# Performance work log

Measured on AMD Instinct MI355X. Metric: run time of the kernel, lower is better.

The kernel has to match this reference:

```python
import jax, jax.numpy as jnp
import numpy as np

D_MODEL = 1024
N_HEADS = 16
HEAD_DIM = D_MODEL // N_HEADS
ROPE_BASE = 10000.0
B, S = 2, 2048


def _rope_cos_sin(seq_len):
    inv_freq = 1.0 / (ROPE_BASE ** (jnp.arange(0, HEAD_DIM, 2, dtype=jnp.float32) / HEAD_DIM))
    t = jnp.arange(seq_len, dtype=jnp.float32)
    freqs = jnp.outer(t, inv_freq)                 # [S, HEAD_DIM/2]
    emb = jnp.concatenate([freqs, freqs], axis=-1)  # [S, HEAD_DIM]
    return jnp.cos(emb), jnp.sin(emb)


def _apply_rope(x, cos, sin):
    # x: [B, H, S, D]; cos/sin: [S, D]
    x1 = x[..., ::2]
    x2 = x[..., 1::2]
    return jnp.concatenate(
        [x1 * cos[..., ::2] - x2 * sin[..., ::2],
         x1 * sin[..., 1::2] + x2 * cos[..., 1::2]], axis=-1)


def setup_inputs() -> dict:
    key = jax.random.key(0)
    ks = jax.random.split(key, 5)
    std = 1.0 / np.sqrt(D_MODEL)
    x = jax.random.normal(ks[0], (B, S, D_MODEL), dtype=jnp.float32)
    Wq = jax.random.normal(ks[1], (D_MODEL, D_MODEL), dtype=jnp.float32) * std
    Wk = jax.random.normal(ks[2], (D_MODEL, D_MODEL), dtype=jnp.float32) * std
    Wv = jax.random.normal(ks[3], (D_MODEL, D_MODEL), dtype=jnp.float32) * std
    Wo = jax.random.normal(ks[4], (D_MODEL, D_MODEL), dtype=jnp.float32) * std
    attn_mask = jnp.tril(jnp.ones((S, S), dtype=jnp.int32))  # 0 = masked (causal)
    return {"x": x, "Wq": Wq, "Wk": Wk, "Wv": Wv, "Wo": Wo, "attn_mask": attn_mask}


def reference(x, Wq, Wk, Wv, Wo, attn_mask):
    b, s, _ = x.shape
    scale = 1.0 / np.sqrt(HEAD_DIM)
    # torch Linear: y = x @ W.T
    q = (x @ Wq.T).reshape(b, s, N_HEADS, HEAD_DIM).transpose(0, 2, 1, 3)
    k = (x @ Wk.T).reshape(b, s, N_HEADS, HEAD_DIM).transpose(0, 2, 1, 3)
    v = (x @ Wv.T).reshape(b, s, N_HEADS, HEAD_DIM).transpose(0, 2, 1, 3)
    cos, sin = _rope_cos_sin(s)
    q = _apply_rope(q, cos, sin)
    k = _apply_rope(k, cos, sin)
    scores = jnp.einsum('bhqd,bhkd->bhqk', q, k) * scale  # [B,H,S,S]
    scores = jnp.where(attn_mask == 0, -jnp.inf, scores)
    attn = jax.nn.softmax(scores, axis=-1)
    out = jnp.einsum('bhqk,bhkd->bhqd', attn, v)
    out = out.transpose(0, 2, 1, 3).reshape(b, s, D_MODEL)
    return out @ Wo.T
```

## Files before the change

### kernel.cpp

```cpp
#include <hip/hip_runtime.h>
#include <hip/hip_bf16.h>
#include <cstdint>

#define SEQ 2048
#define NH  16
#define HD  64
#define DM  1024
#define BATCH 2

typedef unsigned short ushort_t;
typedef __attribute__((ext_vector_type(8))) short short8;
typedef __attribute__((ext_vector_type(4))) float f32x4;

__device__ __forceinline__ ushort_t f2bf(float f){
  __hip_bfloat16 h = __float2bfloat16(f);
  return *reinterpret_cast<ushort_t*>(&h);
}
__device__ __forceinline__ ushort_t f2bf_fast(float f){
  uint32_t u = __float_as_uint(f);
  u += 0x7FFF + ((u >> 16) & 1);
  return (ushort_t)(u >> 16);
}

__global__ __launch_bounds__(256) void rope_tab_kernel(float* __restrict__ tab){
  int idx = blockIdx.x * 256 + threadIdx.x;
  int t = idx >> 5, j = idx & 31;
  float invf = exp2f(-(float)j * 0.41524101186092033f);
  float sn, cn;
  sincosf((float)t * invf, &sn, &cn);
  tab[2*idx]   = cn;
  tab[2*idx+1] = sn;
}

__global__ __launch_bounds__(256) void cvt_kernel(
    const float* __restrict__ x,  const float* __restrict__ Wq,
    const float* __restrict__ Wk, const float* __restrict__ Wv,
    const float* __restrict__ Wo,
    ushort_t* __restrict__ xb,  ushort_t* __restrict__ wqb,
    ushort_t* __restrict__ wkb, ushort_t* __restrict__ wvb,
    ushort_t* __restrict__ wob)
{
  int f = blockIdx.x * 256 + threadIdx.x;
  const float* s; ushort_t* d; int off;
  if(f < (1<<20)){ s = x; d = xb; off = f; }
  else{
    int r = f - (1<<20);
    int w = r >> 18;
    off = r & ((1<<18)-1);
    s = (w==0)?Wq:(w==1)?Wk:(w==2)?Wv:Wo;
    d = (w==0)?wqb:(w==1)?wkb:(w==2)?wvb:wob;
  }
  float4 v = *reinterpret_cast<const float4*>(s + (size_t)off*4);
  ushort_t t[4] = {f2bf(v.x), f2bf(v.y), f2bf(v.z), f2bf(v.w)};
  *reinterpret_cast<uint2*>(d + (size_t)off*4) = *reinterpret_cast<const uint2*>(t);
}

__device__ __forceinline__ void gemm_core_bf16(
    const ushort_t* __restrict__ A, const ushort_t* __restrict__ B,
    ushort_t* As, ushort_t* Bs, int m0, int n0, f32x4 acc[4][4])
{
  const int tid  = threadIdx.x;
  const int lane = tid & 63;
  const int wave = tid >> 6;
  const int quad = lane >> 4, l16 = lane & 15;
  const int wm = (wave >> 1) * 64, wn = (wave & 1) * 64;
  for(int k0 = 0; k0 < DM; k0 += 32){
    #pragma unroll
    for(int u = 0; u < 2; u++){
      int idx = tid + u * 256;
      int row = idx >> 2, seg = idx & 3;
      *reinterpret_cast<uint4*>(&As[row*40 + seg*8]) =
        *reinterpret_cast<const uint4*>(&A[(size_t)(m0+row)*DM + k0 + seg*8]);
      *reinterpret_cast<uint4*>(&Bs[row*40 + seg*8]) =
        *reinterpret_cast<const uint4*>(&B[(size_t)(n0+row)*DM + k0 + seg*8]);
    }
    __syncthreads();
    short8 af[4], bf[4];
    #pragma unroll
    for(int mt=0;mt<4;mt++) af[mt] = *reinterpret_cast<const short8*>(&As[(wm+mt*16+l16)*40 + quad*8]);
    #pragma unroll
    for(int nt=0;nt<4;nt++) bf[nt] = *reinterpret_cast<const short8*>(&Bs[(wn+nt*16+l16)*40 + quad*8]);
    #pragma unroll
    for(int mt=0;mt<4;mt++)
      #pragma unroll
      for(int nt=0;nt<4;nt++)
        acc[mt][nt] = __builtin_amdgcn_mfma_f32_16x16x32_bf16(af[mt], bf[nt], acc[mt][nt], 0, 0, 0);
    __syncthreads();
  }
}
__device__ __forceinline__ void gemm_core_f32(
    const float* __restrict__ A, const float* __restrict__ B,
    ushort_t* As, ushort_t* Bs, int m0, int n0, f32x4 acc[4][4])
{
  const int tid  = threadIdx.x;
  const int lane = tid & 63;
  const int wave = tid >> 6;
  const int quad = lane >> 4, l16 = lane & 15;
  const int wm = (wave >> 1) * 64, wn = (wave & 1) * 64;
  for(int k0 = 0; k0 < DM; k0 += 32){
    #pragma unroll
    for(int u = 0; u < 4; u++){
      int idx = tid + u * 256;
      int row = idx >> 3, seg = idx & 7;
      float4 av = *reinterpret_cast<const float4*>(&A[(size_t)(m0+row)*DM + k0 + seg*4]);
      float4 bv = *reinterpret_cast<const float4*>(&B[(size_t)(n0+row)*DM + k0 + seg*4]);
      ushort_t at[4] = {f2bf(av.x), f2bf(av.y), f2bf(av.z), f2bf(av.w)};
      ushort_t bt[4] = {f2bf(bv.x), f2bf(bv.y), f2bf(bv.z), f2bf(bv.w)};
      *reinterpret_cast<uint2*>(&As[row*40 + seg*4]) = *reinterpret_cast<const uint2*>(at);
      *reinterpret_cast<uint2*>(&Bs[row*40 + seg*4]) = *reinterpret_cast<const uint2*>(bt);
    }
    __syncthreads();
    short8 af[4], bf[4];
    #pragma unroll
    for(int mt=0;mt<4;mt++) af[mt] = *reinterpret_cast<const short8*>(&As[(wm+mt*16+l16)*40 + quad*8]);
    #pragma unroll
    for(int nt=0;nt<4;nt++) bf[nt] = *reinterpret_cast<const short8*>(&Bs[(wn+nt*16+l16)*40 + quad*8]);
    #pragma unroll
    for(int mt=0;mt<4;mt++)
      #pragma unroll
      for(int nt=0;nt<4;nt++)
        acc[mt][nt] = __builtin_amdgcn_mfma_f32_16x16x32_bf16(af[mt], bf[nt], acc[mt][nt], 0, 0, 0);
    __syncthreads();
  }
}

__device__ __forceinline__ void qkv_epilogue(
    int z, int m0, int n0, f32x4 acc[4][4], const float* __restrict__ tab,
    ushort_t* __restrict__ Q, ushort_t* __restrict__ Ko, ushort_t* __restrict__ Vt)
{
  const int tid  = threadIdx.x;
  const int lane = tid & 63;
  const int wave = tid >> 6;
  const int quad = lane >> 4, l16 = lane & 15;
  const int wm = (wave >> 1) * 64, wn = (wave & 1) * 64;
  if(z < 2){
    ushort_t* outp = (z == 0) ? Q : Ko;
    const float qscale = (z == 0) ? 0.125f : 1.0f;
    #pragma unroll
    for(int nt=0;nt<4;nt++){
      int n  = n0 + wn + nt*16 + l16;
      int h  = n >> 6, dh = n & 63;
      int j  = dh & 31;
      int outd = (dh >> 1) + (dh & 1) * 32;
      bool even = (dh & 1) == 0;
      #pragma unroll
      for(int mt=0;mt<4;mt++){
        #pragma unroll
        for(int r=0;r<4;r++){
          int m = m0 + wm + mt*16 + quad*4 + r;
          int b = m >> 11, s = m & 2047;
          float v = acc[mt][nt][r];
          float p = __shfl_xor(v, 1);
          float2 cs = *reinterpret_cast<const float2*>(&tab[(s*32 + j)*2]);
          float o = even ? (v * cs.x - p * cs.y) : (p * cs.y + v * cs.x);
          outp[((size_t)(b*NH + h)*SEQ + s)*HD + outd] = f2bf(o * qscale);
        }
      }
    }
  } else {
    #pragma unroll
    for(int nt=0;nt<4;nt++){
      int n = n0 + wn + nt*16 + l16;
      int h = n >> 6, dh = n & 63;
      #pragma unroll
      for(int mt=0;mt<4;mt++){
        #pragma unroll
        for(int r=0;r<4;r++){
          int m = m0 + wm + mt*16 + quad*4 + r;
          int b = m >> 11, s = m & 2047;
          Vt[((size_t)(b*NH + h)*HD + dh)*SEQ + s] = f2bf(acc[mt][nt][r]);
        }
      }
    }
  }
}

__global__ __launch_bounds__(256) void qkv_bf16_kernel(
    const ushort_t* __restrict__ xb,
    const ushort_t* __restrict__ wqb, const ushort_t* __restrict__ wkb,
    const ushort_t* __restrict__ wvb, const float* __restrict__ tab,
    ushort_t* __restrict__ Q, ushort_t* __restrict__ Ko, ushort_t* __restrict__ Vt)
{
  const int z = blockIdx.z;
  const ushort_t* W = (z == 0) ? wqb : (z == 1) ? wkb : wvb;
  const int m0 = blockIdx.x * 128, n0 = blockIdx.y * 128;
  __shared__ __align__(16) char smem[20480];
  ushort_t* As = (ushort_t*)smem;
  ushort_t* Bs = (ushort_t*)(smem + 10240);
  f32x4 acc[4][4];
  #pragma unroll
  for(int i=0;i<4;i++)
    #pragma unroll
    for(int j=0;j<4;j++) acc[i][j] = (f32x4){0.f,0.f,0.f,0.f};
  gemm_core_bf16(xb, W, As, Bs, m0, n0, acc);
  qkv_epilogue(z, m0, n0, acc, tab, Q, Ko, Vt);
}

__global__ __launch_bounds__(256) void qkv_f32_kernel(
    const float* __restrict__ x,
    const float* __restrict__ Wq, const float* __restrict__ Wk,
    const float* __restrict__ Wv, const float* __restrict__ tab,
    ushort_t* __restrict__ Q, ushort_t* __restrict__ Ko, ushort_t* __restrict__ Vt)
{
  const int z = blockIdx.z;
  const float* W = (z == 0) ? Wq : (z == 1) ? Wk : Wv;
  const int m0 = blockIdx.x * 128, n0 = blockIdx.y * 128;
  __shared__ __align__(16) char smem[20480];
  ushort_t* As = (ushort_t*)smem;
  ushort_t* Bs = (ushort_t*)(smem + 10240);
  f32x4 acc[4][4];
  #pragma unroll
  for(int i=0;i<4;i++)
    #pragma unroll
    for(int j=0;j<4;j++) acc[i][j] = (f32x4){0.f,0.f,0.f,0.f};
  gemm_core_f32(x, W, As, Bs, m0, n0, acc);
  qkv_epilogue(z, m0, n0, acc, tab, Q, Ko, Vt);
}

__global__ __launch_bounds__(256) void attn_kernel(
    ushort_t* __restrict__ Qbuf, const ushort_t* __restrict__ K,
    const ushort_t* __restrict__ Vt)
{
  const int bh = blockIdx.x;
  const int y  = blockIdx.y;
  const int g  = (y < 8) ? (15 - y) : (y - 8);
  const int T  = 2*(g+1);
  const int tid  = threadIdx.x;
  const int lane = tid & 63;
  const int wave = tid >> 6;
  const int quad = lane >> 4, l16 = lane & 15;

  ushort_t*       Qp = Qbuf + (size_t)bh * SEQ * HD;
  const ushort_t* Kp = K    + (size_t)bh * SEQ * HD;
  const ushort_t* Vp = Vt   + (size_t)bh * HD * SEQ;

  __shared__ __align__(16) ushort_t Ks[64*72];
  __shared__ __align__(16) ushort_t Vs[64*72];
  __shared__ __align__(16) ushort_t Pl[4][32*72];
  ushort_t* pl = &Pl[wave][0];

  const int srow0 = tid >> 3;
  const int scol  = (tid & 7) * 8;

  const int q0w = 128*g + 32*wave;

  short8 qf[2][2];
  #pragma unroll
  for(int s=0;s<2;s++)
    #pragma unroll
    for(int kk=0;kk<2;kk++)
      qf[s][kk] = *reinterpret_cast<const short8*>(&Qp[(size_t)(q0w + 16*s + l16)*HD + kk*32 + quad*8]);

  f32x4 oacc[2][4];
  #pragma unroll
  for(int s=0;s<2;s++)
    #pragma unroll
    for(int dt=0;dt<4;dt++) oacc[s][dt] = (f32x4){0.f,0.f,0.f,0.f};
  float llane[2] = {0.f, 0.f};

  uint4 kreg[2], vreg[2];
  #pragma unroll
  for(int u=0;u<2;u++){
    int row = srow0 + u*32;
    kreg[u] = *reinterpret_cast<const uint4*>(&Kp[(size_t)row*HD + scol]);
    vreg[u] = *reinterpret_cast<const uint4*>(&Vp[(size_t)row*SEQ + scol]);
  }

  for(int t = 0; t < T; t++){
    const int kv0 = t * 64;

    __syncthreads();
    #pragma unroll
    for(int u=0;u<2;u++){
      int row = srow0 + u*32;
      *reinterpret_cast<uint4*>(&Ks[row*72 + scol]) = kreg[u];
      *reinterpret_cast<uint4*>(&Vs[row*72 + scol]) = vreg[u];
    }
    __syncthreads();

    if(t < T-1){
      #pragma unroll
      for(int u=0;u<2;u++){
        int row = srow0 + u*32;
        kreg[u] = *reinterpret_cast<const uint4*>(&Kp[(size_t)(kv0 + 64 + row)*HD + scol]);
        vreg[u] = *reinterpret_cast<const uint4*>(&Vp[(size_t)row*SEQ + kv0 + 64 + scol]);
      }
    }

    short8 kf[4][2], vf[4][2];
    #pragma unroll
    for(int nt=0;nt<4;nt++)
      #pragma unroll
      for(int kk=0;kk<2;kk++)
        kf[nt][kk] = *reinterpret_cast<const short8*>(&Ks[(nt*16 + l16)*72 + kk*32 + quad*8]);
    #pragma unroll
    for(int dt=0;dt<4;dt++)
      #pragma unroll
      for(int kk=0;kk<2;kk++)
        vf[dt][kk] = *reinterpret_cast<const short8*>(&Vs[(dt*16 + l16)*72 + kk*32 + quad*8]);

    #pragma unroll
    for(int s=0;s<2;s++){
      f32x4 sacc[4];
      #pragma unroll
      for(int nt=0;nt<4;nt++) sacc[nt] = (f32x4){0.f,0.f,0.f,0.f};
      #pragma unroll
      for(int kk=0;kk<2;kk++)
        #pragma unroll
        for(int nt=0;nt<4;nt++)
          sacc[nt] = __builtin_amdgcn_mfma_f32_16x16x32_bf16(kf[nt][kk], qf[s][kk], sacc[nt], 0,0,0);

      const int q_abs = q0w + 16*s + l16;
      const bool maskable = (kv0 + 63 > q0w + 16*s);
      float pv[4][4];
      #pragma unroll
      for(int nt=0;nt<4;nt++)
        #pragma unroll
        for(int r=0;r<4;r++){
          float sv = sacc[nt][r];
          if(maskable){
            int kv_abs = kv0 + nt*16 + quad*4 + r;
            sv = (kv_abs > q_abs) ? -1e30f : sv;
          }
          float p = __expf(sv);
          pv[nt][r] = p;
          llane[s] += p;
        }

      asm volatile("" ::: "memory");
      #pragma unroll
      for(int nt=0;nt<4;nt++){
        uint32_t lo = (uint32_t)f2bf_fast(pv[nt][0]) | ((uint32_t)f2bf_fast(pv[nt][1]) << 16);
        uint32_t hi = (uint32_t)f2bf_fast(pv[nt][2]) | ((uint32_t)f2bf_fast(pv[nt][3]) << 16);
        uint2 pk; pk.x = lo; pk.y = hi;
        *reinterpret_cast<uint2*>(&pl[(16*s + l16)*72 + nt*16 + quad*4]) = pk;
      }
      asm volatile("s_waitcnt lgkmcnt(0)" ::: "memory");

      #pragma unroll
      for(int kk=0;kk<2;kk++){
        short8 pf = *reinterpret_cast<const short8*>(&pl[(16*s + l16)*72 + kk*32 + quad*8]);
        #pragma unroll
        for(int dt=0;dt<4;dt++)
          oacc[s][dt] = __builtin_amdgcn_mfma_f32_16x16x32_bf16(vf[dt][kk], pf, oacc[s][dt], 0,0,0);
      }
    }
  }

  #pragma unroll
  for(int s=0;s<2;s++){
    float lt = llane[s];
    lt += __shfl_xor(lt, 16);
    lt += __shfl_xor(lt, 32);
    float inv = 1.0f / lt;
    #pragma unroll
    for(int dt=0;dt<4;dt++){
      uint32_t lo = (uint32_t)f2bf_fast(oacc[s][dt][0] * inv) | ((uint32_t)f2bf_fast(oacc[s][dt][1] * inv) << 16);
      uint32_t hi = (uint32_t)f2bf_fast(oacc[s][dt][2] * inv) | ((uint32_t)f2bf_fast(oacc[s][dt][3] * inv) << 16);
      uint2 pk; pk.x = lo; pk.y = hi;
      *reinterpret_cast<uint2*>(&Qp[(size_t)(q0w + 16*s + l16)*HD + dt*16 + quad*4]) = pk;
    }
  }
}

__global__ __launch_bounds__(256) void out_proj_bf16_kernel(
    const ushort_t* __restrict__ ctx, const ushort_t* __restrict__ wob,
    float* __restrict__ out)
{
  const int m0 = blockIdx.x * 128, n0 = blockIdx.y * 128;
  __shared__ __align__(16) ushort_t As[128*40];
  __shared__ __align__(16) ushort_t Bs[128*40];
  const int tid  = threadIdx.x;
  const int lane = tid & 63;
  const int wave = tid >> 6;
  const int quad = lane >> 4, l16 = lane & 15;
  const int wm = (wave >> 1) * 64, wn = (wave & 1) * 64;

  f32x4 acc[4][4];
  #pragma unroll
  for(int i=0;i<4;i++)
    #pragma unroll
    for(int j=0;j<4;j++) acc[i][j] = (f32x4){0.f,0.f,0.f,0.f};

  for(int k0 = 0; k0 < DM; k0 += 32){
    const int head = k0 >> 6, off = k0 & 63;
    #pragma unroll
    for(int u = 0; u < 2; u++){
      int idx = tid + u * 256;
      int row = idx >> 2, seg = idx & 3;
      int m = m0 + row, b = m >> 11, s = m & 2047;
      *reinterpret_cast<uint4*>(&As[row*40 + seg*8]) =
        *reinterpret_cast<const uint4*>(&ctx[((size_t)(b*NH + head)*SEQ + s)*HD + off + seg*8]);
      *reinterpret_cast<uint4*>(&Bs[row*40 + seg*8]) =
        *reinterpret_cast<const uint4*>(&wob[(size_t)(n0+row)*DM + k0 + seg*8]);
    }
    __syncthreads();
    short8 af[4], bf[4];
    #pragma unroll
    for(int mt=0;mt<4;mt++) af[mt] = *reinterpret_cast<const short8*>(&As[(wm+mt*16+l16)*40 + quad*8]);
    #pragma unroll
    for(int nt=0;nt<4;nt++) bf[nt] = *reinterpret_cast<const short8*>(&Bs[(wn+nt*16+l16)*40 + quad*8]);
    #pragma unroll
    for(int mt=0;mt<4;mt++)
      #pragma unroll
      for(int nt=0;nt<4;nt++)
        acc[mt][nt] = __builtin_amdgcn_mfma_f32_16x16x32_bf16(af[mt], bf[nt], acc[mt][nt], 0, 0, 0);
    __syncthreads();
  }
  #pragma unroll
  for(int mt=0;mt<4;mt++)
    #pragma unroll
    for(int nt=0;nt<4;nt++)
      #pragma unroll
      for(int r=0;r<4;r++){
        int m = m0 + wm + mt*16 + quad*4 + r;
        int n = n0 + wn + nt*16 + l16;
        out[(size_t)m*DM + n] = acc[mt][nt][r];
      }
}

__global__ __launch_bounds__(256) void out_proj_f32_kernel(
    const ushort_t* __restrict__ ctx, const float* __restrict__ Wo,
    float* __restrict__ out)
{
  const int m0 = blockIdx.x * 128, n0 = blockIdx.y * 128;
  __shared__ __align__(16) ushort_t As[128*40];
  __shared__ __align__(16) ushort_t Bs[128*40];
  const int tid  = threadIdx.x;
  const int lane = tid & 63;
  const int wave = tid >> 6;
  const int quad = lane >> 4, l16 = lane & 15;
  const int wm = (wave >> 1) * 64, wn = (wave & 1) * 64;

  f32x4 acc[4][4];
  #pragma unroll
  for(int i=0;i<4;i++)
    #pragma unroll
    for(int j=0;j<4;j++) acc[i][j] = (f32x4){0.f,0.f,0.f,0.f};

  for(int k0 = 0; k0 < DM; k0 += 32){
    const int head = k0 >> 6, off = k0 & 63;
    #pragma unroll
    for(int u = 0; u < 2; u++){
      int idx = tid + u * 256;
      int row = idx >> 2, seg = idx & 3;
      int m = m0 + row, b = m >> 11, s = m & 2047;
      *reinterpret_cast<uint4*>(&As[row*40 + seg*8]) =
        *reinterpret_cast<const uint4*>(&ctx[((size_t)(b*NH + head)*SEQ + s)*HD + off + seg*8]);
    }
    #pragma unroll
    for(int u = 0; u < 4; u++){
      int idx = tid + u * 256;
      int row = idx >> 3, seg = idx & 7;
      float4 bv = *reinterpret_cast<const float4*>(&Wo[(size_t)(n0+row)*DM + k0 + seg*4]);
      ushort_t bt[4] = {f2bf(bv.x), f2bf(bv.y), f2bf(bv.z), f2bf(bv.w)};
      *reinterpret_cast<uint2*>(&Bs[row*40 + seg*4]) = *reinterpret_cast<const uint2*>(bt);
    }
    __syncthreads();
    short8 af[4], bf[4];
    #pragma unroll
    for(int mt=0;mt<4;mt++) af[mt] = *reinterpret_cast<const short8*>(&As[(wm+mt*16+l16)*40 + quad*8]);
    #pragma unroll
    for(int nt=0;nt<4;nt++) bf[nt] = *reinterpret_cast<const short8*>(&Bs[(wn+nt*16+l16)*40 + quad*8]);
    #pragma unroll
    for(int mt=0;mt<4;mt++)
      #pragma unroll
      for(int nt=0;nt<4;nt++)
        acc[mt][nt] = __builtin_amdgcn_mfma_f32_16x16x32_bf16(af[mt], bf[nt], acc[mt][nt], 0, 0, 0);
    __syncthreads();
  }
  #pragma unroll
  for(int mt=0;mt<4;mt++)
    #pragma unroll
    for(int nt=0;nt<4;nt++)
      #pragma unroll
      for(int r=0;r<4;r++){
        int m = m0 + wm + mt*16 + quad*4 + r;
        int n = n0 + wn + nt*16 + l16;
        out[(size_t)m*DM + n] = acc[mt][nt][r];
      }
}

extern "C" void kernel_launch(void* const* d_in, const int* in_sizes, int n_in,
                              void* d_out, int out_size, void* d_ws, size_t ws_size,
                              hipStream_t stream) {
  const float* x  = (const float*)d_in[0];
  const float* Wq = (const float*)d_in[1];
  const float* Wk = (const float*)d_in[2];
  const float* Wv = (const float*)d_in[3];
  const float* Wo = (const float*)d_in[4];
  float* out = (float*)d_out;

  char* ws = (char*)d_ws;
  ushort_t* Qb  = (ushort_t*)ws;
  float*    tab = (float*)(ws + (8u << 20));
  ushort_t* Kb  = (ushort_t*)d_out;
  ushort_t* Vt  = (ushort_t*)d_out + (size_t)BATCH*NH*SEQ*HD;

  rope_tab_kernel<<<256, 256, 0, stream>>>(tab);

  const bool big_ws = ws_size >= (25u << 20);

  if(big_ws){
    ushort_t* xb  = (ushort_t*)(ws + (8u  << 20) + (512u << 10));
    char*     wb0 = ws + (16u << 20) + (512u << 10);
    ushort_t* wqb = (ushort_t*)(wb0);
    ushort_t* wkb = (ushort_t*)(wb0 + (2u << 20));
    ushort_t* wvb = (ushort_t*)(wb0 + (4u << 20));
    ushort_t* wob = (ushort_t*)(wb0 + (6u << 20));
    cvt_kernel<<<8192, 256, 0, stream>>>(x, Wq, Wk, Wv, Wo, xb, wqb, wkb, wvb, wob);
    dim3 g1(32, 8, 3);
    qkv_bf16_kernel<<<g1, 256, 0, stream>>>(xb, wqb, wkb, wvb, tab, Qb, Kb, Vt);
    dim3 g2(32, 16);
    attn_kernel<<<g2, 256, 0, stream>>>(Qb, Kb, Vt);
    dim3 g3(32, 8);
    out_proj_bf16_kernel<<<g3, 256, 0, stream>>>(Qb, wob, out);
  } else {
    dim3 g1(32, 8, 3);
    qkv_f32_kernel<<<g1, 256, 0, stream>>>(x, Wq, Wk, Wv, tab, Qb, Kb, Vt);
    dim3 g2(32, 16);
    attn_kernel<<<g2, 256, 0, stream>>>(Qb, Kb, Vt);
    dim3 g3(32, 8);
    out_proj_f32_kernel<<<g3, 256, 0, stream>>>(Qb, Wo, out);
  }
}
```

Baseline: 248.3 us.

## Split-KV attention with balanced pairing of causal query blocks per workgroup

The attention kernel now pairs a long and a short 32-row query block per workgroup and splits their KV tiles evenly across the four waves. Partial outputs and row sums are merged through shared-memory float atomics before normalising and writing back. K/V are read straight from global memory instead of being staged in LDS, exp2f is used with log2e folded into the Q scale, and the grid doubles. The V projection swaps its MFMA operands so the transposed V store is contiguous along the sequence. The aim is to remove causal load imbalance and LDS staging cost, at the price of atomic contention and uncached K/V reloads.

```diff
diff --git a/kernel.cpp b/kernel.cpp
--- a/kernel.cpp
+++ b/kernel.cpp
@@ -55,6 +55,7 @@
   *reinterpret_cast<uint2*>(d + (size_t)off*4) = *reinterpret_cast<const uint2*>(t);
 }
 
+template<bool SWAP>
 __device__ __forceinline__ void gemm_core_bf16(
     const ushort_t* __restrict__ A, const ushort_t* __restrict__ B,
     ushort_t* As, ushort_t* Bs, int m0, int n0, f32x4 acc[4][4])
@@ -84,10 +85,13 @@
     for(int mt=0;mt<4;mt++)
       #pragma unroll
       for(int nt=0;nt<4;nt++)
-        acc[mt][nt] = __builtin_amdgcn_mfma_f32_16x16x32_bf16(af[mt], bf[nt], acc[mt][nt], 0, 0, 0);
-    __syncthreads();
-  }
-}
+        acc[mt][nt] = SWAP
+          ? __builtin_amdgcn_mfma_f32_16x16x32_bf16(bf[nt], af[mt], acc[mt][nt], 0, 0, 0)
+          : __builtin_amdgcn_mfma_f32_16x16x32_bf16(af[mt], bf[nt], acc[mt][nt], 0, 0, 0);
+    __syncthreads();
+  }
+}
+template<bool SWAP>
 __device__ __forceinline__ void gemm_core_f32(
     const float* __restrict__ A, const float* __restrict__ B,
     ushort_t* As, ushort_t* Bs, int m0, int n0, f32x4 acc[4][4])
@@ -119,7 +123,9 @@
     for(int mt=0;mt<4;mt++)
       #pragma unroll
       for(int nt=0;nt<4;nt++)
-        acc[mt][nt] = __builtin_amdgcn_mfma_f32_16x16x32_bf16(af[mt], bf[nt], acc[mt][nt], 0, 0, 0);
+        acc[mt][nt] = SWAP
+          ? __builtin_amdgcn_mfma_f32_16x16x32_bf16(bf[nt], af[mt], acc[mt][nt], 0, 0, 0)
+          : __builtin_amdgcn_mfma_f32_16x16x32_bf16(af[mt], bf[nt], acc[mt][nt], 0, 0, 0);
     __syncthreads();
   }
 }
@@ -135,7 +141,7 @@
   const int wm = (wave >> 1) * 64, wn = (wave & 1) * 64;
   if(z < 2){
     ushort_t* outp = (z == 0) ? Q : Ko;
-    const float qscale = (z == 0) ? 0.125f : 1.0f;
+    const float qscale = (z == 0) ? 0.18033688011112042f : 1.0f;
     #pragma unroll
     for(int nt=0;nt<4;nt++){
       int n  = n0 + wn + nt*16 + l16;
@@ -160,15 +166,15 @@
   } else {
     #pragma unroll
     for(int nt=0;nt<4;nt++){
-      int n = n0 + wn + nt*16 + l16;
-      int h = n >> 6, dh = n & 63;
       #pragma unroll
       for(int mt=0;mt<4;mt++){
+        int m = m0 + wm + mt*16 + l16;
+        int b = m >> 11, s = m & 2047;
         #pragma unroll
         for(int r=0;r<4;r++){
-          int m = m0 + wm + mt*16 + quad*4 + r;
-          int b = m >> 11, s = m & 2047;
-          Vt[((size_t)(b*NH + h)*HD + dh)*SEQ + s] = f2bf(acc[mt][nt][r]);
+          int n = n0 + wn + nt*16 + quad*4 + r;
+          int h = n >> 6, dh = n & 63;
+          Vt[((size_t)(b*NH + h)*HD + dh)*SEQ + s] = f2bf_fast(acc[mt][nt][r]);
         }
       }
     }
@@ -192,7 +198,8 @@
   for(int i=0;i<4;i++)
     #pragma unroll
     for(int j=0;j<4;j++) acc[i][j] = (f32x4){0.f,0.f,0.f,0.f};
-  gemm_core_bf16(xb, W, As, Bs, m0, n0, acc);
+  if(z == 2) gemm_core_bf16<true >(xb, W, As, Bs, m0, n0, acc);
+  else       gemm_core_bf16<false>(xb, W, As, Bs, m0, n0, acc);
   qkv_epilogue(z, m0, n0, acc, tab, Q, Ko, Vt);
 }
 
@@ -213,18 +220,19 @@
   for(int i=0;i<4;i++)
     #pragma unroll
     for(int j=0;j<4;j++) acc[i][j] = (f32x4){0.f,0.f,0.f,0.f};
-  gemm_core_f32(x, W, As, Bs, m0, n0, acc);
+  if(z == 2) gemm_core_f32<true >(x, W, As, Bs, m0, n0, acc);
+  else       gemm_core_f32<false>(x, W, As, Bs, m0, n0, acc);
   qkv_epilogue(z, m0, n0, acc, tab, Q, Ko, Vt);
 }
 
-__global__ __launch_bounds__(256) void attn_kernel(
+__global__ __launch_bounds__(256, 4) void attn_kernel(
     ushort_t* __restrict__ Qbuf, const ushort_t* __restrict__ K,
     const ushort_t* __restrict__ Vt)
 {
   const int bh = blockIdx.x;
-  const int y  = blockIdx.y;
-  const int g  = (y < 8) ? (15 - y) : (y - 8);
-  const int T  = 2*(g+1);
+  const int pr = blockIdx.y;
+  const int jb = 63 - pr;
+  const int Tb = (jb >> 1) + 1;
   const int tid  = threadIdx.x;
   const int lane = tid & 63;
   const int wave = tid >> 6;
@@ -234,132 +242,143 @@
   const ushort_t* Kp = K    + (size_t)bh * SEQ * HD;
   const ushort_t* Vp = Vt   + (size_t)bh * HD * SEQ;
 
-  __shared__ __align__(16) ushort_t Ks[64*72];
-  __shared__ __align__(16) ushort_t Vs[64*72];
+  __shared__ float part_o[2][32*HD];
+  __shared__ float part_l[2][32];
   __shared__ __align__(16) ushort_t Pl[4][32*72];
   ushort_t* pl = &Pl[wave][0];
 
-  const int srow0 = tid >> 3;
-  const int scol  = (tid & 7) * 8;
-
-  const int q0w = 128*g + 32*wave;
-
-  short8 qf[2][2];
-  #pragma unroll
-  for(int s=0;s<2;s++)
-    #pragma unroll
-    for(int kk=0;kk<2;kk++)
-      qf[s][kk] = *reinterpret_cast<const short8*>(&Qp[(size_t)(q0w + 16*s + l16)*HD + kk*32 + quad*8]);
-
-  f32x4 oacc[2][4];
-  #pragma unroll
-  for(int s=0;s<2;s++)
-    #pragma unroll
-    for(int dt=0;dt<4;dt++) oacc[s][dt] = (f32x4){0.f,0.f,0.f,0.f};
-  float llane[2] = {0.f, 0.f};
-
-  uint4 kreg[2], vreg[2];
-  #pragma unroll
-  for(int u=0;u<2;u++){
-    int row = srow0 + u*32;
-    kreg[u] = *reinterpret_cast<const uint4*>(&Kp[(size_t)row*HD + scol]);
-    vreg[u] = *reinterpret_cast<const uint4*>(&Vp[(size_t)row*SEQ + scol]);
-  }
-
-  for(int t = 0; t < T; t++){
-    const int kv0 = t * 64;
-
-    __syncthreads();
-    #pragma unroll
-    for(int u=0;u<2;u++){
-      int row = srow0 + u*32;
-      *reinterpret_cast<uint4*>(&Ks[row*72 + scol]) = kreg[u];
-      *reinterpret_cast<uint4*>(&Vs[row*72 + scol]) = vreg[u];
-    }
-    __syncthreads();
-
-    if(t < T-1){
-      #pragma unroll
-      for(int u=0;u<2;u++){
-        int row = srow0 + u*32;
-        kreg[u] = *reinterpret_cast<const uint4*>(&Kp[(size_t)(kv0 + 64 + row)*HD + scol]);
-        vreg[u] = *reinterpret_cast<const uint4*>(&Vp[(size_t)row*SEQ + kv0 + 64 + scol]);
+  for (int i = tid; i < 2*32*HD; i += 256) (&part_o[0][0])[i] = 0.f;
+  if (tid < 64) (&part_l[0][0])[tid] = 0.f;
+  __syncthreads();
+
+  int slot = (wave * 33) >> 2;
+  const int send_ = ((wave + 1) * 33) >> 2;
+
+  while (slot < send_) {
+    int qb, sel, t0, ntile;
+    if (slot < Tb) {
+      qb = jb; sel = 0; t0 = slot;
+      int e = (send_ < Tb) ? send_ : Tb;
+      ntile = e - slot; slot = e;
+    } else {
+      qb = pr; sel = 1; t0 = slot - Tb;
+      ntile = send_ - slot; slot = send_;
+    }
+
+    short8 qf[2][2];
+    #pragma unroll
+    for (int s = 0; s < 2; s++)
+      #pragma unroll
+      for (int kk = 0; kk < 2; kk++)
+        qf[s][kk] = *reinterpret_cast<const short8*>(
+            &Qp[(size_t)(qb*32 + 16*s + l16)*HD + kk*32 + quad*8]);
+
+    f32x4 oacc[2][4];
+    #pragma unroll
+    for (int s = 0; s < 2; s++)
+      #pragma unroll
+      for (int dt = 0; dt < 4; dt++) oacc[s][dt] = (f32x4){0.f,0.f,0.f,0.f};
+    float llane[2] = {0.f, 0.f};
+
+    for (int tt = 0; tt < ntile; tt++) {
+      const int kv0 = (t0 + tt) * 64;
+
+      short8 kf[4][2];
+      #pragma unroll
+      for (int nt = 0; nt < 4; nt++)
+        #pragma unroll
+        for (int kk = 0; kk < 2; kk++)
+          kf[nt][kk] = *reinterpret_cast<const short8*>(
+              &Kp[(size_t)(kv0 + nt*16 + l16)*HD + kk*32 + quad*8]);
+
+      f32x4 sacc[2][4];
+      #pragma unroll
+      for (int s = 0; s < 2; s++)
+        #pragma unroll
+        for (int nt = 0; nt < 4; nt++) sacc[s][nt] = (f32x4){0.f,0.f,0.f,0.f};
+      #pragma unroll
+      for (int s = 0; s < 2; s++)
+        #pragma unroll
+        for (int kk = 0; kk < 2; kk++)
+          #pragma unroll
+          for (int nt = 0; nt < 4; nt++)
+            sacc[s][nt] = __builtin_amdgcn_mfma_f32_16x16x32_bf16(
+                kf[nt][kk], qf[s][kk], sacc[s][nt], 0,0,0);
+
+      short8 vf[4][2];
+      #pragma unroll
+      for (int dt = 0; dt < 4; dt++)
+        #pragma unroll
+        for (int kk = 0; kk < 2; kk++)
+          vf[dt][kk] = *reinterpret_cast<const short8*>(
+              &Vp[(size_t)(dt*16 + l16)*SEQ + kv0 + kk*32 + quad*8]);
+
+      #pragma unroll
+      for (int s = 0; s < 2; s++) {
+        const int q_abs = qb*32 + 16*s + l16;
+        const bool maskable = (kv0 + 63 > qb*32 + 16*s);
+        #pragma unroll
+        for (int nt = 0; nt < 4; nt++)
+          #pragma unroll
+          for (int r = 0; r < 4; r++) {
+            float sv = sacc[s][nt][r];
+            if (maskable) {
+              int kv_abs = kv0 + nt*16 + quad*4 + r;
+              sv = (kv_abs > q_abs) ? -1e30f : sv;
+            }
+            float pe = exp2f(sv);
+            sacc[s][nt][r] = pe;
+            llane[s] += pe;
+          }
       }
-    }
-
-    short8 kf[4][2], vf[4][2];
-    #pragma unroll
-    for(int nt=0;nt<4;nt++)
-      #pragma unroll
-      for(int kk=0;kk<2;kk++)
-        kf[nt][kk] = *reinterpret_cast<const short8*>(&Ks[(nt*16 + l16)*72 + kk*32 + quad*8]);
-    #pragma unroll
-    for(int dt=0;dt<4;dt++)
-      #pragma unroll
-      for(int kk=0;kk<2;kk++)
-        vf[dt][kk] = *reinterpret_cast<const short8*>(&Vs[(dt*16 + l16)*72 + kk*32 + quad*8]);
-
-    #pragma unroll
-    for(int s=0;s<2;s++){
-      f32x4 sacc[4];
-      #pragma unroll
-      for(int nt=0;nt<4;nt++) sacc[nt] = (f32x4){0.f,0.f,0.f,0.f};
-      #pragma unroll
-      for(int kk=0;kk<2;kk++)
-        #pragma unroll
-        for(int nt=0;nt<4;nt++)
-          sacc[nt] = __builtin_amdgcn_mfma_f32_16x16x32_bf16(kf[nt][kk], qf[s][kk], sacc[nt], 0,0,0);
-
-      const int q_abs = q0w + 16*s + l16;
-      const bool maskable = (kv0 + 63 > q0w + 16*s);
-      float pv[4][4];
-      #pragma unroll
-      for(int nt=0;nt<4;nt++)
-        #pragma unroll
-        for(int r=0;r<4;r++){
-          float sv = sacc[nt][r];
-          if(maskable){
-            int kv_abs = kv0 + nt*16 + quad*4 + r;
-            sv = (kv_abs > q_abs) ? -1e30f : sv;
-          }
-          float p = __expf(sv);
-          pv[nt][r] = p;
-          llane[s] += p;
+
+      asm volatile("" ::: "memory");
+      #pragma unroll
+      for (int s = 0; s < 2; s++)
+        #pragma unroll
+        for (int nt = 0; nt < 4; nt++) {
+          uint32_t lo = (uint32_t)f2bf_fast(sacc[s][nt][0]) | ((uint32_t)f2bf_fast(sacc[s][nt][1]) << 16);
+          uint32_t hi = (uint32_t)f2bf_fast(sacc[s][nt][2]) | ((uint32_t)f2bf_fast(sacc[s][nt][3]) << 16);
+          uint2 pk; pk.x = lo; pk.y = hi;
+          *reinterpret_cast<uint2*>(&pl[(16*s + l16)*72 + nt*16 + quad*4]) = pk;
         }
-
-      asm volatile("" ::: "memory");
-      #pragma unroll
-      for(int nt=0;nt<4;nt++){
-        uint32_t lo = (uint32_t)f2bf_fast(pv[nt][0]) | ((uint32_t)f2bf_fast(pv[nt][1]) << 16);
-        uint32_t hi = (uint32_t)f2bf_fast(pv[nt][2]) | ((uint32_t)f2bf_fast(pv[nt][3]) << 16);
-        uint2 pk; pk.x = lo; pk.y = hi;
-        *reinterpret_cast<uint2*>(&pl[(16*s + l16)*72 + nt*16 + quad*4]) = pk;
-      }
       asm volatile("s_waitcnt lgkmcnt(0)" ::: "memory");
 
       #pragma unroll
-      for(int kk=0;kk<2;kk++){
-        short8 pf = *reinterpret_cast<const short8*>(&pl[(16*s + l16)*72 + kk*32 + quad*8]);
-        #pragma unroll
-        for(int dt=0;dt<4;dt++)
-          oacc[s][dt] = __builtin_amdgcn_mfma_f32_16x16x32_bf16(vf[dt][kk], pf, oacc[s][dt], 0,0,0);
-      }
-    }
-  }
-
-  #pragma unroll
-  for(int s=0;s<2;s++){
-    float lt = llane[s];
-    lt += __shfl_xor(lt, 16);
-    lt += __shfl_xor(lt, 32);
-    float inv = 1.0f / lt;
-    #pragma unroll
-    for(int dt=0;dt<4;dt++){
-      uint32_t lo = (uint32_t)f2bf_fast(oacc[s][dt][0] * inv) | ((uint32_t)f2bf_fast(oacc[s][dt][1] * inv) << 16);
-      uint32_t hi = (uint32_t)f2bf_fast(oacc[s][dt][2] * inv) | ((uint32_t)f2bf_fast(oacc[s][dt][3] * inv) << 16);
-      uint2 pk; pk.x = lo; pk.y = hi;
-      *reinterpret_cast<uint2*>(&Qp[(size_t)(q0w + 16*s + l16)*HD + dt*16 + quad*4]) = pk;
-    }
+      for (int s = 0; s < 2; s++)
+        #pragma unroll
+        for (int kk = 0; kk < 2; kk++) {
+          short8 pf = *reinterpret_cast<const short8*>(&pl[(16*s + l16)*72 + kk*32 + quad*8]);
+          #pragma unroll
+          for (int dt = 0; dt < 4; dt++)
+            oacc[s][dt] = __builtin_amdgcn_mfma_f32_16x16x32_bf16(
+                vf[dt][kk], pf, oacc[s][dt], 0,0,0);
+        }
+    }
+
+    #pragma unroll
+    for (int s = 0; s < 2; s++) {
+      atomicAdd(&part_l[sel][16*s + l16], llane[s]);
+      #pragma unroll
+      for (int dt = 0; dt < 4; dt++)
+        #pragma unroll
+        for (int r = 0; r < 4; r++)
+          atomicAdd(&part_o[sel][(16*s + l16)*HD + dt*16 + quad*4 + r], oacc[s][dt][r]);
+    }
+  }
+  __syncthreads();
+
+  for (int c = tid; c < 512; c += 256) {
+    int sel = c >> 8;
+    int q   = (c >> 3) & 31;
+    int d0  = (c & 7) * 8;
+    int qb  = sel ? pr : jb;
+    float inv = 1.0f / part_l[sel][q];
+    ushort_t tmp[8];
+    #pragma unroll
+    for (int e = 0; e < 8; e++)
+      tmp[e] = f2bf_fast(part_o[sel][q*HD + d0 + e] * inv);
+    *reinterpret_cast<uint4*>(&Qp[(size_t)(qb*32 + q)*HD + d0]) = *reinterpret_cast<const uint4*>(tmp);
   }
 }
 
@@ -511,14 +530,14 @@
     cvt_kernel<<<8192, 256, 0, stream>>>(x, Wq, Wk, Wv, Wo, xb, wqb, wkb, wvb, wob);
     dim3 g1(32, 8, 3);
     qkv_bf16_kernel<<<g1, 256, 0, stream>>>(xb, wqb, wkb, wvb, tab, Qb, Kb, Vt);
-    dim3 g2(32, 16);
+    dim3 g2(32, 32);
     attn_kernel<<<g2, 256, 0, stream>>>(Qb, Kb, Vt);
     dim3 g3(32, 8);
     out_proj_bf16_kernel<<<g3, 256, 0, stream>>>(Qb, wob, out);
   } else {
     dim3 g1(32, 8, 3);
     qkv_f32_kernel<<<g1, 256, 0, stream>>>(x, Wq, Wk, Wv, tab, Qb, Kb, Vt);
-    dim3 g2(32, 16);
+    dim3 g2(32, 32);
     attn_kernel<<<g2, 256, 0, stream>>>(Qb, Kb, Vt);
     dim3 g3(32, 8);
     out_proj_f32_kernel<<<g3, 256, 0, stream>>>(Qb, Wo, out);
```

Result: slower. 313.5 us (+26.2%).

## Use direct global-to-LDS loads with XOR swizzle; swap MFMA operands for V

Applied to the files above, without the earlier changes.

Replaces register-staged global→LDS copies in the bf16 QKV GEMM and the output-projection GEMM with global_load_lds direct loads. The padded LDS rows are replaced by an XOR-swizzled 32-element layout to avoid bank conflicts. For the V projection the MFMA operands are swapped so each lane holds consecutive sequence positions, which changes the transposed V store pattern. The log2(e) factor is folded into the Q scale so softmax can use exp2f instead of __expf. The trade-off is more complex addressing and reliance on the LDS-load builtin's wave-uniform base semantics.

```diff
diff --git a/kernel.cpp b/kernel.cpp
--- a/kernel.cpp
+++ b/kernel.cpp
@@ -21,6 +21,10 @@
   u += 0x7FFF + ((u >> 16) & 1);
   return (ushort_t)(u >> 16);
 }
+
+#define GLDS(g, l) __builtin_amdgcn_global_load_lds( \
+    (const __attribute__((address_space(1))) void*)(g), \
+    (__attribute__((address_space(3))) void*)(l), 16, 0, 0)
 
 __global__ __launch_bounds__(256) void rope_tab_kernel(float* __restrict__ tab){
   int idx = blockIdx.x * 256 + threadIdx.x;
@@ -55,7 +59,8 @@
   *reinterpret_cast<uint2*>(d + (size_t)off*4) = *reinterpret_cast<const uint2*>(t);
 }
 
-__device__ __forceinline__ void gemm_core_bf16(
+template<bool SWAP>
+__device__ __forceinline__ void gemm_core_bf16_glds(
     const ushort_t* __restrict__ A, const ushort_t* __restrict__ B,
     ushort_t* As, ushort_t* Bs, int m0, int n0, f32x4 acc[4][4])
 {
@@ -69,25 +74,36 @@
     for(int u = 0; u < 2; u++){
       int idx = tid + u * 256;
       int row = idx >> 2, seg = idx & 3;
-      *reinterpret_cast<uint4*>(&As[row*40 + seg*8]) =
-        *reinterpret_cast<const uint4*>(&A[(size_t)(m0+row)*DM + k0 + seg*8]);
-      *reinterpret_cast<uint4*>(&Bs[row*40 + seg*8]) =
-        *reinterpret_cast<const uint4*>(&B[(size_t)(n0+row)*DM + k0 + seg*8]);
+      int col = (seg ^ (row & 3)) * 8;
+      ushort_t* la = &As[(size_t)(idx & ~63) * 8];
+      ushort_t* lb = &Bs[(size_t)(idx & ~63) * 8];
+      GLDS(&A[(size_t)(m0+row)*DM + k0 + col], la);
+      GLDS(&B[(size_t)(n0+row)*DM + k0 + col], lb);
     }
     __syncthreads();
     short8 af[4], bf[4];
     #pragma unroll
-    for(int mt=0;mt<4;mt++) af[mt] = *reinterpret_cast<const short8*>(&As[(wm+mt*16+l16)*40 + quad*8]);
-    #pragma unroll
-    for(int nt=0;nt<4;nt++) bf[nt] = *reinterpret_cast<const short8*>(&Bs[(wn+nt*16+l16)*40 + quad*8]);
+    for(int mt=0;mt<4;mt++){
+      int row = wm + mt*16 + l16;
+      af[mt] = *reinterpret_cast<const short8*>(&As[row*32 + (quad ^ (row&3))*8]);
+    }
+    #pragma unroll
+    for(int nt=0;nt<4;nt++){
+      int row = wn + nt*16 + l16;
+      bf[nt] = *reinterpret_cast<const short8*>(&Bs[row*32 + (quad ^ (row&3))*8]);
+    }
     #pragma unroll
     for(int mt=0;mt<4;mt++)
       #pragma unroll
       for(int nt=0;nt<4;nt++)
-        acc[mt][nt] = __builtin_amdgcn_mfma_f32_16x16x32_bf16(af[mt], bf[nt], acc[mt][nt], 0, 0, 0);
-    __syncthreads();
-  }
-}
+        acc[mt][nt] = SWAP
+          ? __builtin_amdgcn_mfma_f32_16x16x32_bf16(bf[nt], af[mt], acc[mt][nt], 0, 0, 0)
+          : __builtin_amdgcn_mfma_f32_16x16x32_bf16(af[mt], bf[nt], acc[mt][nt], 0, 0, 0);
+    __syncthreads();
+  }
+}
+
+template<bool SWAP>
 __device__ __forceinline__ void gemm_core_f32(
     const float* __restrict__ A, const float* __restrict__ B,
     ushort_t* As, ushort_t* Bs, int m0, int n0, f32x4 acc[4][4])
@@ -119,7 +135,9 @@
     for(int mt=0;mt<4;mt++)
       #pragma unroll
       for(int nt=0;nt<4;nt++)
-        acc[mt][nt] = __builtin_amdgcn_mfma_f32_16x16x32_bf16(af[mt], bf[nt], acc[mt][nt], 0, 0, 0);
+        acc[mt][nt] = SWAP
+          ? __builtin_amdgcn_mfma_f32_16x16x32_bf16(bf[nt], af[mt], acc[mt][nt], 0, 0, 0)
+          : __builtin_amdgcn_mfma_f32_16x16x32_bf16(af[mt], bf[nt], acc[mt][nt], 0, 0, 0);
     __syncthreads();
   }
 }
@@ -135,7 +153,7 @@
   const int wm = (wave >> 1) * 64, wn = (wave & 1) * 64;
   if(z < 2){
     ushort_t* outp = (z == 0) ? Q : Ko;
-    const float qscale = (z == 0) ? 0.125f : 1.0f;
+    const float qscale = (z == 0) ? 0.18033688011112042f : 1.0f;
     #pragma unroll
     for(int nt=0;nt<4;nt++){
       int n  = n0 + wn + nt*16 + l16;
@@ -160,15 +178,15 @@
   } else {
     #pragma unroll
     for(int nt=0;nt<4;nt++){
-      int n = n0 + wn + nt*16 + l16;
-      int h = n >> 6, dh = n & 63;
       #pragma unroll
       for(int mt=0;mt<4;mt++){
+        int m = m0 + wm + mt*16 + l16;
+        int b = m >> 11, s = m & 2047;
         #pragma unroll
         for(int r=0;r<4;r++){
-          int m = m0 + wm + mt*16 + quad*4 + r;
-          int b = m >> 11, s = m & 2047;
-          Vt[((size_t)(b*NH + h)*HD + dh)*SEQ + s] = f2bf(acc[mt][nt][r]);
+          int n = n0 + wn + nt*16 + quad*4 + r;
+          int h = n >> 6, dh = n & 63;
+          Vt[((size_t)(b*NH + h)*HD + dh)*SEQ + s] = f2bf_fast(acc[mt][nt][r]);
         }
       }
     }
@@ -184,15 +202,15 @@
   const int z = blockIdx.z;
   const ushort_t* W = (z == 0) ? wqb : (z == 1) ? wkb : wvb;
   const int m0 = blockIdx.x * 128, n0 = blockIdx.y * 128;
-  __shared__ __align__(16) char smem[20480];
-  ushort_t* As = (ushort_t*)smem;
-  ushort_t* Bs = (ushort_t*)(smem + 10240);
+  __shared__ __align__(16) ushort_t As[128*32];
+  __shared__ __align__(16) ushort_t Bs[128*32];
   f32x4 acc[4][4];
   #pragma unroll
   for(int i=0;i<4;i++)
     #pragma unroll
     for(int j=0;j<4;j++) acc[i][j] = (f32x4){0.f,0.f,0.f,0.f};
-  gemm_core_bf16(xb, W, As, Bs, m0, n0, acc);
+  if(z == 2) gemm_core_bf16_glds<true >(xb, W, As, Bs, m0, n0, acc);
+  else       gemm_core_bf16_glds<false>(xb, W, As, Bs, m0, n0, acc);
   qkv_epilogue(z, m0, n0, acc, tab, Q, Ko, Vt);
 }
 
@@ -213,7 +231,8 @@
   for(int i=0;i<4;i++)
     #pragma unroll
     for(int j=0;j<4;j++) acc[i][j] = (f32x4){0.f,0.f,0.f,0.f};
-  gemm_core_f32(x, W, As, Bs, m0, n0, acc);
+  if(z == 2) gemm_core_f32<true >(x, W, As, Bs, m0, n0, acc);
+  else       gemm_core_f32<false>(x, W, As, Bs, m0, n0, acc);
   qkv_epilogue(z, m0, n0, acc, tab, Q, Ko, Vt);
 }
 
@@ -322,7 +341,7 @@
             int kv_abs = kv0 + nt*16 + quad*4 + r;
             sv = (kv_abs > q_abs) ? -1e30f : sv;
           }
-          float p = __expf(sv);
+          float p = exp2f(sv);
           pv[nt][r] = p;
           llane[s] += p;
         }
@@ -368,8 +387,8 @@
     float* __restrict__ out)
 {
   const int m0 = blockIdx.x * 128, n0 = blockIdx.y * 128;
-  __shared__ __align__(16) ushort_t As[128*40];
-  __shared__ __align__(16) ushort_t Bs[128*40];
+  __shared__ __align__(16) ushort_t As[128*32];
+  __shared__ __align__(16) ushort_t Bs[128*32];
   const int tid  = threadIdx.x;
   const int lane = tid & 63;
   const int wave = tid >> 6;
@@ -388,18 +407,25 @@
     for(int u = 0; u < 2; u++){
       int idx = tid + u * 256;
       int row = idx >> 2, seg = idx & 3;
+      int col = (seg ^ (row & 3)) * 8;
       int m = m0 + row, b = m >> 11, s = m & 2047;
-      *reinterpret_cast<uint4*>(&As[row*40 + seg*8]) =
-        *reinterpret_cast<const uint4*>(&ctx[((size_t)(b*NH + head)*SEQ + s)*HD + off + seg*8]);
-      *reinterpret_cast<uint4*>(&Bs[row*40 + seg*8]) =
-        *reinterpret_cast<const uint4*>(&wob[(size_t)(n0+row)*DM + k0 + seg*8]);
+      ushort_t* la = &As[(size_t)(idx & ~63) * 8];
+      ushort_t* lb = &Bs[(size_t)(idx & ~63) * 8];
+      GLDS(&ctx[((size_t)(b*NH + head)*SEQ + s)*HD + off + col], la);
+      GLDS(&wob[(size_t)(n0+row)*DM + k0 + col], lb);
     }
     __syncthreads();
     short8 af[4], bf[4];
     #pragma unroll
-    for(int mt=0;mt<4;mt++) af[mt] = *reinterpret_cast<const short8*>(&As[(wm+mt*16+l16)*40 + quad*8]);
-    #pragma unroll
-    for(int nt=0;nt<4;nt++) bf[nt] = *reinterpret_cast<const short8*>(&Bs[(wn+nt*16+l16)*40 + quad*8]);
+    for(int mt=0;mt<4;mt++){
+      int row = wm + mt*16 + l16;
+      af[mt] = *reinterpret_cast<const short8*>(&As[row*32 + (quad ^ (row&3))*8]);
+    }
+    #pragma unroll
+    for(int nt=0;nt<4;nt++){
+      int row = wn + nt*16 + l16;
+      bf[nt] = *reinterpret_cast<const short8*>(&Bs[row*32 + (quad ^ (row&3))*8]);
+    }
     #pragma unroll
     for(int mt=0;mt<4;mt++)
       #pragma unroll
```

Measured after the change: 253.9 us. +2.2%, slower.
